# Kernel optimization log

Hardware: AMD Instinct MI355X
Metric: run time of the kernel (lower is better)

## Reference

```python
import math
import jax, jax.numpy as jnp
import numpy as np
from jax import lax

B, T, D = 2, 2048, 1024
H, W, E = 16, 16, 8
HD = D // H


def setup_inputs() -> dict:
    key = jax.random.key(0)
    ks = jax.random.split(key, 9)
    s = 0.02
    return {
        "x": jax.random.normal(ks[0], (B, T, D), dtype=jnp.float32),
        # CausalConv1d weights: torch Conv1d layout [out_ch, in_ch, kernel]
        "q_w": jax.random.normal(ks[1], (D, D, W), dtype=jnp.float32) * s,
        "q_b": jax.random.normal(ks[2], (D,), dtype=jnp.float32) * s,
        "k_w": jax.random.normal(ks[3], (D, D, W), dtype=jnp.float32) * s,
        "k_b": jax.random.normal(ks[4], (D,), dtype=jnp.float32) * s,
        # Linear weights: torch layout [out, in]
        "v_w": jax.random.normal(ks[5], (D, D), dtype=jnp.float32) * s,
        "v_b": jax.random.normal(ks[6], (D,), dtype=jnp.float32) * s,
        "p_w": jax.random.normal(ks[7], (D, D), dtype=jnp.float32) * s,
        "p_b": jax.random.normal(ks[8], (D,), dtype=jnp.float32) * s,
    }


def _causal_conv(x_t, w, b):
    # x_t: [B, D, T]; left-pad by W-1 so output at t sees inputs <= t
    xp = jnp.pad(x_t, ((0, 0), (0, 0), (W - 1, 0)))
    y = lax.conv_general_dilated(xp, w, window_strides=(1,), padding="VALID",
                                 dimension_numbers=("NCH", "OIH", "NCH"))
    return y + b[None, :, None]


def _split_heads(z):
    # [B, T, D] -> [B, H, T, hd]
    return z.reshape(B, T, H, HD).transpose(0, 2, 1, 3)


def reference(x, q_w, q_b, k_w, k_b, v_w, v_b, p_w, p_b):
    x_t = x.transpose(0, 2, 1)  # [B, D, T]
    q = _split_heads(_causal_conv(x_t, q_w, q_b).transpose(0, 2, 1))
    k = _split_heads(_causal_conv(x_t, k_w, k_b).transpose(0, 2, 1))
    v = _split_heads(jnp.einsum("btd,od->bto", x, v_w) + v_b)
    scale = 1.0 / math.sqrt(HD)

    # ---- local window attention (unfold equivalent) ----
    # zero-pad keys/values W-1 steps to the left along T, gather sliding windows
    k_pad = jnp.pad(k, ((0, 0), (0, 0), (W - 1, 0), (0, 0)))
    v_pad = jnp.pad(v, ((0, 0), (0, 0), (W - 1, 0), (0, 0)))
    widx = jnp.arange(T)[:, None] + jnp.arange(W)[None, :]  # [T, W]
    patches_k = k_pad[:, :, widx]  # [B, H, T, W, hd]
    patches_v = v_pad[:, :, widx]  # [B, H, T, W, hd]
    attn_l = jax.nn.softmax(jnp.einsum("bhtd,bhtwd->bhtw", q, patches_k) * scale, axis=-1)
    out_l = jnp.einsum("bhtw,bhtwd->bhtd", attn_l, patches_v)

    # ---- exponential jumps: roll by 2^e (wrap-around, as in original) ----
    out_e = jnp.zeros_like(out_l)
    for e in range(E):
        shift = 2 ** e
        if shift >= T:
            break
        k_s = jnp.roll(k, -shift, axis=2)
        v_s = jnp.roll(v, -shift, axis=2)
        score = jnp.sum(q * k_s, axis=-1) * scale  # [B, H, T]
        alpha = jax.nn.softmax(score, axis=-1)[..., None]  # softmax over T (faithful)
        out_e = out_e + alpha * v_s

    out = (out_l + out_e).transpose(0, 2, 1, 3).reshape(B, T, D)
    return jnp.einsum("btd,od->bto", out, p_w) + p_b
```

## Files before the change

kernel.cpp:

```cpp
#include <hip/hip_runtime.h>
#include <cstdint>
#include <cstddef>

#define TSEQ 2048
#define DDIM 1024

typedef _Float16 f16;
typedef _Float16 f16x2 __attribute__((ext_vector_type(2)));
typedef _Float16 f16x4 __attribute__((ext_vector_type(4)));
typedef _Float16 f16x8 __attribute__((ext_vector_type(8)));
typedef float f32x4 __attribute__((ext_vector_type(4)));


__device__ __align__(16) static const unsigned char g_zero16[16] = {};

__device__ __forceinline__ void gload_lds16(const void* g, void* l) {
  __builtin_amdgcn_global_load_lds(
      (const __attribute__((address_space(1))) void*)g,
      (__attribute__((address_space(3))) void*)l, 16, 0, 0);
}

__global__ void cvt_all(const float* __restrict__ x, const float* __restrict__ vw,
                        const float* __restrict__ pw,
                        f16* __restrict__ xh, f16* __restrict__ vwh, f16* __restrict__ pwh) {
  int b = blockIdx.x;
  const float* src; f16* dst; int i;
  if (b < 4096)      { src = x;  dst = xh;  i = b * 256 + threadIdx.x; }
  else if (b < 5120) { src = vw; dst = vwh; i = (b - 4096) * 256 + threadIdx.x; }
  else               { src = pw; dst = pwh; i = (b - 5120) * 256 + threadIdx.x; }
  float4 v = ((const float4*)src)[i];
  f16x4 h = { (f16)v.x, (f16)v.y, (f16)v.z, (f16)v.w };
  ((f16x4*)dst)[i] = h;
}

__global__ __launch_bounds__(256) void cvt_w_frag(const float* __restrict__ qw,
                                                  const float* __restrict__ kw,
                                                  f16* __restrict__ qd, f16* __restrict__ kd) {
  extern __shared__ f16 wt_lds[];
  const int bid = blockIdx.x;
  const int proj = bid >> 9;
  const int nb = (bid >> 5) & 15;
  const int j = (bid >> 3) & 3;
  const int ic = bid & 7;
  const float* src = proj ? kw : qw;
  f16* dst = proj ? kd : qd;
  const int o_base = nb * 64 + j * 16;
  const int tid = threadIdx.x;
  const int lane = tid & 63;
  const int wv = tid >> 6;

  #pragma unroll
  for (int p = 0; p < 32; p++) {
    const int gidx = p * 256 + tid;
    const int o_r = gidx >> 9;
    const int i_r = (gidx >> 2) & 127;
    const int wq2 = gidx & 3;
    float4 v = *(const float4*)(src + (size_t)(o_base + o_r) * 16384 +
                                (size_t)(ic * 128 + i_r) * 16 + wq2 * 4);
    const int g = i_r >> 3;
    const int gp = (g & 8) | ((g & 7) ^ (o_r & 7));
    const int ip = gp * 8 + (i_r & 7);
    f16* t0 = wt_lds + ((wq2 * 4) * 16 + o_r) * 130 + ip;
    t0[0]    = (f16)v.x;
    t0[2080] = (f16)v.y;
    t0[4160] = (f16)v.z;
    t0[6240] = (f16)v.w;
  }
  __syncthreads();

  const int o = lane & 15;
  const int lhi = lane >> 4;
  #pragma unroll
  for (int u4 = 0; u4 < 16; u4++) {
    const int u = u4 * 4 + wv;
    const int w = u >> 2, ih = (u >> 1) & 1, s = u & 1;
    const int gl = ih * 8 + s * 4 + lhi;
    const int gp = (gl & 8) | ((gl & 7) ^ (o & 7));
    f16x8 val = *(const f16x8*)&wt_lds[(w * 16 + o) * 130 + gp * 8];
    const size_t unit = ((size_t)(nb * 256 + (ic * 2 + ih) * 16 + w) * 8) + j * 2 + s;
    *(f16x8*)(dst + unit * 512 + lane * 8) = val;
  }
}

__global__ __launch_bounds__(512, 1) void gemm_qk8(
    const f16* __restrict__ xh,
    const f16* __restrict__ Wfq, const f16* __restrict__ Wfk,
    const float* __restrict__ bq, const float* __restrict__ bk,
    f16* __restrict__ oq, f16* __restrict__ ok)
{
  extern __shared__ __align__(16) f16 smem[];
  const int tid = threadIdx.x;
  const int lane = tid & 63;
  const int wid = tid >> 6;
  const int wq = wid >> 1;
  const int wp = wid & 1;

  const int flat = blockIdx.y * 16 + blockIdx.x;
  const int xcd = flat & 7;
  const int idx = flat >> 3;
  const int nblk = xcd * 2 + (idx >> 4);
  const int mblk = idx & 15;
  const int m0 = mblk * 256;
  const int n0 = nblk * 64;
  const int bT = m0 & ~(TSEQ - 1);
  const int t0 = m0 & (TSEQ - 1);

  const int srow = lane >> 3;
  const int chunk8 = (((lane & 7) ^ (srow & 7)) << 3);

  const f16* Wf = wp ? Wfk : Wfq;
  const f16* wbase = Wf + ((size_t)nblk << 20) + lane * 8;

  f32x4 acc[4][4] = {};
  f16x8 bfr[2][8];
  f16x8 afr[2][8];

  auto stageX = [&](int ib2, int bufp) {
    f16* sb = smem + bufp * 17408;
    const int ic = ib2 * 64 + chunk8;
    #pragma unroll
    for (int c = 0; c < 5; c++) {
      const int g = c * 8 + wid;
      if (g < 34) {
        const int srcT = t0 + g * 8 + srow - 15;
        const void* gp = (srcT >= 0)
            ? (const void*)(xh + (((size_t)(bT + srcT)) << 10) + ic)
            : (const void*)g_zero16;
        gload_lds16(gp, (void*)&sb[g * 512]);
      }
    }
  };

  auto loadB = [&](int kt, f16x8* bf) {
    const f16* p = wbase + ((size_t)kt << 12);
    #pragma unroll
    for (int f = 0; f < 8; f++)
      bf[f] = *(const f16x8*)(p + f * 512);
  };

  auto readA = [&](const f16* xb, int wt, f16x8* af) {
    const int rx = ((lane & 7) + wt) & 7;
    const int sl0 = (((lane >> 4)) ^ rx) << 3;
    const int sl1 = (((lane >> 4) + 4) ^ rx) << 3;
    #pragma unroll
    for (int i = 0; i < 4; i++) {
      const int row = wq * 64 + i * 16 + (lane & 15) + wt;
      af[i]     = *(const f16x8*)&xb[row * 64 + sl0];
      af[4 + i] = *(const f16x8*)&xb[row * 64 + sl1];
    }
  };

  stageX(0, 0);
  loadB(0, bfr[0]);
  asm volatile("s_waitcnt vmcnt(0)" ::: "memory");
  __builtin_amdgcn_s_barrier();
  __builtin_amdgcn_sched_barrier(0);

  for (int ib = 0; ib < 16; ib++) {
    if (ib > 0) {
      __builtin_amdgcn_s_barrier();
      __builtin_amdgcn_sched_barrier(0);
    }
    if (ib + 1 < 16) stageX(ib + 1, (ib + 1) & 1);
    __builtin_amdgcn_sched_barrier(0);
    const f16* xb = smem + (ib & 1) * 17408;
    readA(xb, 0, afr[0]);
    #pragma unroll
    for (int wt = 0; wt < 16; wt++) {
      if (wt < 15) readA(xb, wt + 1, afr[(wt + 1) & 1]);
      const int kt = ib * 16 + wt;
      if (kt + 1 < 256) loadB(kt + 1, bfr[(wt & 1) ^ 1]);
      __builtin_amdgcn_s_setprio(1);
      #pragma unroll
      for (int i = 0; i < 4; i++)
        #pragma unroll
        for (int j = 0; j < 4; j++)
          acc[i][j] = __builtin_amdgcn_mfma_f32_16x16x32_f16(
              afr[wt & 1][i], bfr[wt & 1][2 * j], acc[i][j], 0, 0, 0);
      #pragma unroll
      for (int i = 0; i < 4; i++)
        #pragma unroll
        for (int j = 0; j < 4; j++)
          acc[i][j] = __builtin_amdgcn_mfma_f32_16x16x32_f16(
              afr[wt & 1][4 + i], bfr[wt & 1][2 * j + 1], acc[i][j], 0, 0, 0);
      __builtin_amdgcn_s_setprio(0);
    }
  }

  const int crow = (lane >> 4) << 2;
  const int ccol = lane & 15;
  const int hh = n0 >> 6;
  const float* bias = wp ? bk : bq;
  f16* outp = wp ? ok : oq;
  #pragma unroll
  for (int j = 0; j < 4; j++) {
    const int col = n0 + j * 16 + ccol;
    const float bvl = bias[col];
    const int d = (j << 4) + ccol;
    #pragma unroll
    for (int i = 0; i < 4; i++) {
      #pragma unroll
      for (int r = 0; r < 4; r++) {
        const int row = m0 + wq * 64 + i * 16 + crow + r;
        const int b = row >> 11, t = row & (TSEQ - 1);
        outp[((size_t)(b * 16 + hh) * TSEQ + t) * 64 + d] = (f16)(acc[i][j][r] + bvl);
      }
    }
  }
}

template<int MODE>
__global__ __launch_bounds__(256, 2) void gemm_small(
    const f16* __restrict__ A, const f16* __restrict__ Bw,
    const float* __restrict__ bias, f16* __restrict__ oh, float* __restrict__ ofp)
{
  __shared__ f16 As[128 * 32];
  __shared__ f16 Bs[128 * 32];
  const int tid = threadIdx.x;
  const int lane = tid & 63;
  const int wid = tid >> 6;
  const int m0 = blockIdx.x * 128;
  const int n0 = blockIdx.y * 128;

  const int srow = lane >> 2;
  const int scg = ((lane & 3) ^ ((lane >> 3) & 3)) * 8;
  const int wm = wid & 1;
  const int wn = wid >> 1;

  f32x4 acc[4][4] = {};

  for (int kk = 0; kk < 1024; kk += 32) {
    __syncthreads();
    if (wid < 2) {
      #pragma unroll
      for (int c = 0; c < 4; c++) {
        const int r = wid * 64 + c * 16 + srow;
        const void* g = (const void*)(A + (((size_t)(m0 + r)) << 10) + kk + scg);
        gload_lds16(g, (void*)&As[(wid * 64 + c * 16) * 32]);
      }
    } else {
      #pragma unroll
      for (int c = 0; c < 4; c++) {
        const int r = (wid - 2) * 64 + c * 16 + srow;
        const void* g = (const void*)(Bw + (((size_t)(n0 + r)) << 10) + kk + scg);
        gload_lds16(g, (void*)&Bs[((wid - 2) * 64 + c * 16) * 32]);
      }
    }
    __syncthreads();
    const int koff = ((lane >> 4) ^ ((lane >> 1) & 3)) * 8;
    f16x8 af[4], bf[4];
    #pragma unroll
    for (int i = 0; i < 4; i++) {
      af[i] = *(const f16x8*)&As[(wm * 64 + i * 16 + (lane & 15)) * 32 + koff];
      bf[i] = *(const f16x8*)&Bs[(wn * 64 + i * 16 + (lane & 15)) * 32 + koff];
    }
    #pragma unroll
    for (int i = 0; i < 4; i++)
      #pragma unroll
      for (int j = 0; j < 4; j++)
        acc[i][j] = __builtin_amdgcn_mfma_f32_16x16x32_f16(af[i], bf[j], acc[i][j], 0, 0, 0);
  }

  const int crow = (lane >> 4) * 4;
  const int ccol = lane & 15;
  #pragma unroll
  for (int j = 0; j < 4; j++) {
    const int col = n0 + wn * 64 + j * 16 + ccol;
    const float bvl = bias[col];
    #pragma unroll
    for (int i = 0; i < 4; i++) {
      #pragma unroll
      for (int r = 0; r < 4; r++) {
        const int row = m0 + wm * 64 + i * 16 + crow + r;
        const float val = acc[i][j][r] + bvl;
        if (MODE == 1) {
          ofp[(size_t)row * DDIM + col] = val;
        } else {
          const int b = row >> 11, t = row & (TSEQ - 1);
          const int h = col >> 6, d = col & 63;
          oh[((size_t)(b * 16 + h) * TSEQ + t) * 64 + d] = (f16)val;
        }
      }
    }
  }
}

__global__ __launch_bounds__(256) void score_k(const f16* __restrict__ qh,
                                               const f16* __restrict__ kh,
                                               float* __restrict__ scores) {
  const int bid = blockIdx.x;
  const int bh = bid >> 5, tc = bid & 31;
  const int tid = threadIdx.x;
  const int wave = tid >> 6, lane = tid & 63;
  const int tr = lane >> 3, dc = lane & 7;
  const size_t base = ((size_t)bh) << 17;
  const f16* qb = qh + base;
  const f16* kb = kh + base;

  #pragma unroll
  for (int p = 0; p < 2; p++) {
    const int t = tc * 64 + p * 32 + wave * 8 + tr;
    f16x8 qv = *(const f16x8*)(qb + (size_t)t * 64 + dc * 8);
    const f16x2* qp = (const f16x2*)&qv;
    #pragma unroll
    for (int e = 0; e < 8; e++) {
      const int ts = (t + (1 << e)) & (TSEQ - 1);
      f16x8 kv = *(const f16x8*)(kb + (size_t)ts * 64 + dc * 8);
      const f16x2* kp = (const f16x2*)&kv;
      float s = 0.f;
      #pragma unroll
      for (int j = 0; j < 4; j++) s = __builtin_amdgcn_fdot2(qp[j], kp[j], s, false);
      s += __shfl_xor(s, 1, 64);
      s += __shfl_xor(s, 2, 64);
      s += __shfl_xor(s, 4, 64);
      if (dc == 0) scores[((size_t)(bh * 8 + e) << 11) + t] = s * 0.125f;
    }
  }
}

__global__ void softmax_k(float* __restrict__ scores) {
  __shared__ float red[4];
  int row = blockIdx.x;
  float* p = scores + ((size_t)row << 11);
  int tid = threadIdx.x;
  float v[8];
  float4 a = ((const float4*)p)[tid * 2];
  float4 b = ((const float4*)p)[tid * 2 + 1];
  v[0] = a.x; v[1] = a.y; v[2] = a.z; v[3] = a.w;
  v[4] = b.x; v[5] = b.y; v[6] = b.z; v[7] = b.w;
  float m = v[0];
  #pragma unroll
  for (int j = 1; j < 8; j++) m = fmaxf(m, v[j]);
  for (int o = 32; o > 0; o >>= 1) m = fmaxf(m, __shfl_xor(m, o, 64));
  if ((tid & 63) == 0) red[tid >> 6] = m;
  __syncthreads();
  m = fmaxf(fmaxf(red[0], red[1]), fmaxf(red[2], red[3]));
  __syncthreads();
  float s = 0.f;
  #pragma unroll
  for (int j = 0; j < 8; j++) { v[j] = __expf(v[j] - m); s += v[j]; }
  for (int o = 32; o > 0; o >>= 1) s += __shfl_xor(s, o, 64);
  if ((tid & 63) == 0) red[tid >> 6] = s;
  __syncthreads();
  s = (red[0] + red[1]) + (red[2] + red[3]);
  float inv = 1.0f / s;
  float4 o1 = make_float4(v[0] * inv, v[1] * inv, v[2] * inv, v[3] * inv);
  float4 o2 = make_float4(v[4] * inv, v[5] * inv, v[6] * inv, v[7] * inv);
  ((float4*)p)[tid * 2] = o1;
  ((float4*)p)[tid * 2 + 1] = o2;
}

__global__ __launch_bounds__(256) void attn_out_k(
    const f16* __restrict__ qh, const f16* __restrict__ kh, const f16* __restrict__ vh,
    const float* __restrict__ alpha, f16* __restrict__ outh)
{
  __shared__ f16 qL[64 * 64];
  __shared__ f16 kL[80 * 64];
  __shared__ f16 vL[208 * 64];
  __shared__ float scL[64 * 16];
  __shared__ float aL[8 * 64];
  const int bh = blockIdx.x, tc = blockIdx.y;
  const int t0 = tc * 64;
  const int tid = threadIdx.x;
  const size_t base = ((size_t)bh) << 17;

  for (int idx = tid; idx < 64 * 8; idx += 256) {
    int r = idx >> 3, c = idx & 7, sl = c ^ (r & 7);
    *(uint4*)&qL[r * 64 + sl * 8] = *(const uint4*)(qh + base + (size_t)(t0 + r) * 64 + c * 8);
  }
  for (int idx = tid; idx < 79 * 8; idx += 256) {
    int r = idx >> 3, c = idx & 7, sl = c ^ (r & 7);
    int g = t0 - 15 + r;
    uint4 val = (g < 0) ? make_uint4(0, 0, 0, 0)
                        : *(const uint4*)(kh + base + (size_t)g * 64 + c * 8);
    *(uint4*)&kL[r * 64 + sl * 8] = val;
  }
  for (int idx = tid; idx < 207 * 8; idx += 256) {
    int r = idx >> 3, c = idx & 7, sl = c ^ (r & 7);
    int g = t0 - 15 + r;
    uint4 val;
    if (g < 0) val = make_uint4(0, 0, 0, 0);
    else {
      if (g >= TSEQ) g -= TSEQ;
      val = *(const uint4*)(vh + base + (size_t)g * 64 + c * 8);
    }
    *(uint4*)&vL[r * 64 + sl * 8] = val;
  }
  for (int idx = tid; idx < 512; idx += 256) {
    int e = idx >> 6, i = idx & 63;
    aL[e * 64 + i] = alpha[((size_t)(bh * 8 + e) << 11) + t0 + i];
  }
  __syncthreads();

  {
    const int tl = tid & 63;
    const int wg = tid >> 6;
    f16x8 qv[8];
    #pragma unroll
    for (int c = 0; c < 8; c++) qv[c] = *(const f16x8*)&qL[tl * 64 + ((c ^ (tl & 7)) * 8)];
    const f16x2* qp = (const f16x2*)&qv[0];
    #pragma unroll
    for (int wi = 0; wi < 4; wi++) {
      const int w = wg * 4 + wi;
      const int r = tl + w;
      float s = 0.f;
      #pragma unroll
      for (int c = 0; c < 8; c++) {
        f16x8 kv = *(const f16x8*)&kL[r * 64 + ((c ^ (r & 7)) * 8)];
        const f16x2* kp = (const f16x2*)&kv;
        #pragma unroll
        for (int j = 0; j < 4; j++) s = __builtin_amdgcn_fdot2(qp[c * 4 + j], kp[j], s, false);
      }
      scL[tl * 16 + w] = s * 0.125f;
    }
  }
  __syncthreads();

  if (tid < 64) {
    float sc[16];
    float m = -1e30f;
    #pragma unroll
    for (int w = 0; w < 16; w++) { sc[w] = scL[tid * 16 + w]; m = fmaxf(m, sc[w]); }
    float sum = 0.f;
    #pragma unroll
    for (int w = 0; w < 16; w++) { sc[w] = __expf(sc[w] - m); sum += sc[w]; }
    float inv = 1.0f / sum;
    #pragma unroll
    for (int w = 0; w < 16; w++) scL[tid * 16 + w] = sc[w] * inv;
  }
  __syncthreads();

  {
    const int tl = tid >> 2;
    const int qd = tid & 3;
    float accv[16] = {};
    #pragma unroll
    for (int w = 0; w < 16; w++) {
      const float pw_ = scL[tl * 16 + w];
      const int r = tl + w;
      #pragma unroll
      for (int c2 = 0; c2 < 2; c2++) {
        const int c = qd * 2 + c2;
        f16x8 v = *(const f16x8*)&vL[r * 64 + ((c ^ (r & 7)) * 8)];
        #pragma unroll
        for (int j = 0; j < 8; j++) accv[c2 * 8 + j] += pw_ * (float)v[j];
      }
    }
    #pragma unroll
    for (int e = 0; e < 8; e++) {
      const float a = aL[e * 64 + tl];
      const int r = tl + 15 + (1 << e);
      #pragma unroll
      for (int c2 = 0; c2 < 2; c2++) {
        const int c = qd * 2 + c2;
        f16x8 v = *(const f16x8*)&vL[r * 64 + ((c ^ (r & 7)) * 8)];
        #pragma unroll
        for (int j = 0; j < 8; j++) accv[c2 * 8 + j] += a * (float)v[j];
      }
    }
    const int b = bh >> 4, h = bh & 15;
    f16* orow = outh + ((size_t)(b * TSEQ + t0 + tl)) * DDIM + h * 64 + qd * 16;
    #pragma unroll
    for (int c2 = 0; c2 < 2; c2++) {
      f16x8 v;
      #pragma unroll
      for (int j = 0; j < 8; j++) v[j] = (f16)accv[c2 * 8 + j];
      *(f16x8*)(orow + c2 * 8) = v;
    }
  }
}

extern "C" void kernel_launch(void* const* d_in, const int* in_sizes, int n_in,
                              void* d_out, int out_size, void* d_ws, size_t ws_size,
                              hipStream_t stream) {
  (void)in_sizes; (void)n_in; (void)out_size; (void)ws_size;
  const float* x   = (const float*)d_in[0];
  const float* q_w = (const float*)d_in[1];
  const float* q_b = (const float*)d_in[2];
  const float* k_w = (const float*)d_in[3];
  const float* k_b = (const float*)d_in[4];
  const float* v_w = (const float*)d_in[5];
  const float* v_b = (const float*)d_in[6];
  const float* p_w = (const float*)d_in[7];
  const float* p_b = (const float*)d_in[8];
  float* out = (float*)d_out;

  char* ws = (char*)d_ws;
  f16* xh      = (f16*)(ws);
  f16* qwh     = (f16*)(ws + 8388608);
  f16* kwh     = (f16*)(ws + 41943040);
  f16* vwh     = (f16*)(ws + 75497472);
  f16* pwh     = (f16*)(ws + 77594624);
  f16* qh      = (f16*)(ws + 79691776);
  f16* kh      = (f16*)(ws + 88080384);
  f16* vh      = (f16*)(ws + 96468992);
  f16* outh    = (f16*)(ws + 104857600);
  float* alpha = (float*)(ws + 113246208);

  static int s_attr_done = 0;
  if (!s_attr_done) {
    hipFuncSetAttribute((const void*)gemm_qk8,
                        hipFuncAttributeMaxDynamicSharedMemorySize, 69632);
    hipFuncSetAttribute((const void*)cvt_w_frag,
                        hipFuncAttributeMaxDynamicSharedMemorySize, 66560);
    s_attr_done = 1;
  }

  cvt_all<<<6144, 256, 0, stream>>>(x, v_w, p_w, xh, vwh, pwh);
  cvt_w_frag<<<1024, 256, 66560, stream>>>(q_w, k_w, qwh, kwh);

  gemm_qk8<<<dim3(16, 16), 512, 69632, stream>>>(xh, qwh, kwh, q_b, k_b, qh, kh);
  gemm_small<0><<<dim3(32, 8), 256, 0, stream>>>(xh, vwh, v_b, vh, nullptr);

  score_k<<<1024, 256, 0, stream>>>(qh, kh, alpha);
  softmax_k<<<256, 256, 0, stream>>>(alpha);
  attn_out_k<<<dim3(32, 32), 256, 0, stream>>>(qh, kh, vh, alpha, outh);

  gemm_small<1><<<dim3(32, 8), 256, 0, stream>>>(outh, pwh, p_b, nullptr, out);
}
```

Measured before the change: 509.2 us.

## Fuse V projection into QK conv GEMM and double-buffer small GEMM

Computes the V linear projection inside the Q/K causal-conv GEMM. It reuses the already-staged x tile at the tap-15 (zero-shift) window, using V weights pre-swizzled into fragment order by a new conversion kernel. This removes the separate V GEMM launch and its re-read of x, at the cost of extra accumulator registers and extra MFMAs on the Q-path waves. The remaining small GEMM (output projection) now double-buffers its LDS tiles to overlap global loads with MFMA.

```diff
diff --git a/kernel.cpp b/kernel.cpp
--- a/kernel.cpp
+++ b/kernel.cpp
@@ -20,17 +20,35 @@
       (__attribute__((address_space(3))) void*)l, 16, 0, 0);
 }
 
-__global__ void cvt_all(const float* __restrict__ x, const float* __restrict__ vw,
-                        const float* __restrict__ pw,
-                        f16* __restrict__ xh, f16* __restrict__ vwh, f16* __restrict__ pwh) {
+__global__ void cvt_all(const float* __restrict__ x, const float* __restrict__ pw,
+                        f16* __restrict__ xh, f16* __restrict__ pwh) {
   int b = blockIdx.x;
   const float* src; f16* dst; int i;
-  if (b < 4096)      { src = x;  dst = xh;  i = b * 256 + threadIdx.x; }
-  else if (b < 5120) { src = vw; dst = vwh; i = (b - 4096) * 256 + threadIdx.x; }
-  else               { src = pw; dst = pwh; i = (b - 5120) * 256 + threadIdx.x; }
+  if (b < 4096) { src = x;  dst = xh;  i = b * 256 + threadIdx.x; }
+  else          { src = pw; dst = pwh; i = (b - 4096) * 256 + threadIdx.x; }
   float4 v = ((const float4*)src)[i];
   f16x4 h = { (f16)v.x, (f16)v.y, (f16)v.z, (f16)v.w };
   ((f16x4*)dst)[i] = h;
+}
+
+__global__ __launch_bounds__(256) void cvt_vw_frag(const float* __restrict__ vw,
+                                                   f16* __restrict__ dst) {
+  const int nb = blockIdx.x >> 4, ib = blockIdx.x & 15;
+  const int tid = threadIdx.x;
+  #pragma unroll
+  for (int h = 0; h < 2; h++) {
+    const int u = h * 256 + tid;
+    const int f = u >> 6, l = u & 63;
+    const int j = f >> 1, s = f & 1;
+    const int o = nb * 64 + j * 16 + (l & 15);
+    const int i0 = ib * 64 + s * 32 + (l >> 4) * 8;
+    const float* p = vw + (size_t)o * 1024 + i0;
+    float4 a = *(const float4*)p;
+    float4 b = *(const float4*)(p + 4);
+    f16x8 v = { (f16)a.x, (f16)a.y, (f16)a.z, (f16)a.w,
+                (f16)b.x, (f16)b.y, (f16)b.z, (f16)b.w };
+    *(f16x8*)(dst + ((size_t)((nb * 16 + ib) * 8 + f)) * 512 + l * 8) = v;
+  }
 }
 
 __global__ __launch_bounds__(256) void cvt_w_frag(const float* __restrict__ qw,
@@ -84,9 +102,9 @@
 
 __global__ __launch_bounds__(512, 1) void gemm_qk8(
     const f16* __restrict__ xh,
-    const f16* __restrict__ Wfq, const f16* __restrict__ Wfk,
-    const float* __restrict__ bq, const float* __restrict__ bk,
-    f16* __restrict__ oq, f16* __restrict__ ok)
+    const f16* __restrict__ Wfq, const f16* __restrict__ Wfk, const f16* __restrict__ Wfv,
+    const float* __restrict__ bq, const float* __restrict__ bk, const float* __restrict__ bv,
+    f16* __restrict__ oq, f16* __restrict__ ok, f16* __restrict__ ov)
 {
   extern __shared__ __align__(16) f16 smem[];
   const int tid = threadIdx.x;
@@ -110,10 +128,13 @@
 
   const f16* Wf = wp ? Wfk : Wfq;
   const f16* wbase = Wf + ((size_t)nblk << 20) + lane * 8;
+  const f16* vbase = Wfv + ((size_t)nblk << 16) + lane * 8;
 
   f32x4 acc[4][4] = {};
+  f32x4 vacc[4][4] = {};
   f16x8 bfr[2][8];
   f16x8 afr[2][8];
+  f16x8 vf[8];
 
   auto stageX = [&](int ib2, int bufp) {
     f16* sb = smem + bufp * 17408;
@@ -138,6 +159,13 @@
       bf[f] = *(const f16x8*)(p + f * 512);
   };
 
+  auto loadV = [&](int ib2, f16x8* bf) {
+    const f16* p = vbase + ((size_t)ib2 << 12);
+    #pragma unroll
+    for (int f = 0; f < 8; f++)
+      bf[f] = *(const f16x8*)(p + f * 512);
+  };
+
   auto readA = [&](const f16* xb, int wt, f16x8* af) {
     const int rx = ((lane & 7) + wt) & 7;
     const int sl0 = (((lane >> 4)) ^ rx) << 3;
@@ -170,6 +198,7 @@
       if (wt < 15) readA(xb, wt + 1, afr[(wt + 1) & 1]);
       const int kt = ib * 16 + wt;
       if (kt + 1 < 256) loadB(kt + 1, bfr[(wt & 1) ^ 1]);
+      if (wt == 15 && wp == 0) loadV(ib, vf);
       __builtin_amdgcn_s_setprio(1);
       #pragma unroll
       for (int i = 0; i < 4; i++)
@@ -184,6 +213,22 @@
           acc[i][j] = __builtin_amdgcn_mfma_f32_16x16x32_f16(
               afr[wt & 1][4 + i], bfr[wt & 1][2 * j + 1], acc[i][j], 0, 0, 0);
       __builtin_amdgcn_s_setprio(0);
+      if (wt == 15 && wp == 0) {
+        __builtin_amdgcn_s_setprio(1);
+        #pragma unroll
+        for (int i = 0; i < 4; i++)
+          #pragma unroll
+          for (int j = 0; j < 4; j++)
+            vacc[i][j] = __builtin_amdgcn_mfma_f32_16x16x32_f16(
+                afr[1][i], vf[2 * j], vacc[i][j], 0, 0, 0);
+        #pragma unroll
+        for (int i = 0; i < 4; i++)
+          #pragma unroll
+          for (int j = 0; j < 4; j++)
+            vacc[i][j] = __builtin_amdgcn_mfma_f32_16x16x32_f16(
+                afr[1][4 + i], vf[2 * j + 1], vacc[i][j], 0, 0, 0);
+        __builtin_amdgcn_s_setprio(0);
+      }
     }
   }
 
@@ -207,6 +252,23 @@
       }
     }
   }
+  if (wp == 0) {
+    #pragma unroll
+    for (int j = 0; j < 4; j++) {
+      const int col = n0 + j * 16 + ccol;
+      const float bvl = bv[col];
+      const int d = (j << 4) + ccol;
+      #pragma unroll
+      for (int i = 0; i < 4; i++) {
+        #pragma unroll
+        for (int r = 0; r < 4; r++) {
+          const int row = m0 + wq * 64 + i * 16 + crow + r;
+          const int b = row >> 11, t = row & (TSEQ - 1);
+          ov[((size_t)(b * 16 + hh) * TSEQ + t) * 64 + d] = (f16)(vacc[i][j][r] + bvl);
+        }
+      }
+    }
+  }
 }
 
 template<int MODE>
@@ -214,8 +276,8 @@
     const f16* __restrict__ A, const f16* __restrict__ Bw,
     const float* __restrict__ bias, f16* __restrict__ oh, float* __restrict__ ofp)
 {
-  __shared__ f16 As[128 * 32];
-  __shared__ f16 Bs[128 * 32];
+  __shared__ f16 As[2][128 * 32];
+  __shared__ f16 Bs[2][128 * 32];
   const int tid = threadIdx.x;
   const int lane = tid & 63;
   const int wid = tid >> 6;
@@ -229,36 +291,46 @@
 
   f32x4 acc[4][4] = {};
 
-  for (int kk = 0; kk < 1024; kk += 32) {
-    __syncthreads();
+  auto stage = [&](int kk, int buf) {
     if (wid < 2) {
       #pragma unroll
       for (int c = 0; c < 4; c++) {
         const int r = wid * 64 + c * 16 + srow;
         const void* g = (const void*)(A + (((size_t)(m0 + r)) << 10) + kk + scg);
-        gload_lds16(g, (void*)&As[(wid * 64 + c * 16) * 32]);
+        gload_lds16(g, (void*)&As[buf][(wid * 64 + c * 16) * 32]);
       }
     } else {
       #pragma unroll
       for (int c = 0; c < 4; c++) {
         const int r = (wid - 2) * 64 + c * 16 + srow;
         const void* g = (const void*)(Bw + (((size_t)(n0 + r)) << 10) + kk + scg);
-        gload_lds16(g, (void*)&Bs[((wid - 2) * 64 + c * 16) * 32]);
-      }
-    }
-    __syncthreads();
+        gload_lds16(g, (void*)&Bs[buf][((wid - 2) * 64 + c * 16) * 32]);
+      }
+    }
+  };
+
+  stage(0, 0);
+  asm volatile("s_waitcnt vmcnt(0)" ::: "memory");
+  __syncthreads();
+
+  int buf = 0;
+  for (int it = 0; it < 32; it++) {
+    if (it + 1 < 32) stage((it + 1) * 32, buf ^ 1);
     const int koff = ((lane >> 4) ^ ((lane >> 1) & 3)) * 8;
     f16x8 af[4], bf[4];
     #pragma unroll
     for (int i = 0; i < 4; i++) {
-      af[i] = *(const f16x8*)&As[(wm * 64 + i * 16 + (lane & 15)) * 32 + koff];
-      bf[i] = *(const f16x8*)&Bs[(wn * 64 + i * 16 + (lane & 15)) * 32 + koff];
+      af[i] = *(const f16x8*)&As[buf][(wm * 64 + i * 16 + (lane & 15)) * 32 + koff];
+      bf[i] = *(const f16x8*)&Bs[buf][(wn * 64 + i * 16 + (lane & 15)) * 32 + koff];
     }
     #pragma unroll
     for (int i = 0; i < 4; i++)
       #pragma unroll
       for (int j = 0; j < 4; j++)
         acc[i][j] = __builtin_amdgcn_mfma_f32_16x16x32_f16(af[i], bf[j], acc[i][j], 0, 0, 0);
+    asm volatile("s_waitcnt vmcnt(0)" ::: "memory");
+    __syncthreads();
+    buf ^= 1;
   }
 
   const int crow = (lane >> 4) * 4;
@@ -506,11 +578,12 @@
     s_attr_done = 1;
   }
 
-  cvt_all<<<6144, 256, 0, stream>>>(x, v_w, p_w, xh, vwh, pwh);
+  cvt_all<<<5120, 256, 0, stream>>>(x, p_w, xh, pwh);
+  cvt_vw_frag<<<256, 256, 0, stream>>>(v_w, vwh);
   cvt_w_frag<<<1024, 256, 66560, stream>>>(q_w, k_w, qwh, kwh);
 
-  gemm_qk8<<<dim3(16, 16), 512, 69632, stream>>>(xh, qwh, kwh, q_b, k_b, qh, kh);
-  gemm_small<0><<<dim3(32, 8), 256, 0, stream>>>(xh, vwh, v_b, vh, nullptr);
+  gemm_qk8<<<dim3(16, 16), 512, 69632, stream>>>(xh, qwh, kwh, vwh,
+                                                 q_b, k_b, v_b, qh, kh, vh);
 
   score_k<<<1024, 256, 0, stream>>>(qh, kh, alpha);
   softmax_k<<<256, 256, 0, stream>>>(alpha);
```

Measured after the change: 619.1 us. 1.22x slower.

## Double-buffer LDS in small GEMM and drop A-fragment prefetch in conv GEMM

Applied to the files above, without the earlier changes.

The small V/P projection GEMM gains a second LDS buffer, so the next K-tile is loaded directly to LDS while MFMAs run on the current one, with a single barrier per iteration instead of two. The conv GEMM stops prefetching A fragments one step ahead into a double register buffer and reads them from LDS just before use. This lowers register pressure, but the LDS read latency is now exposed to the compiler's scheduling. Doubling the LDS in the small GEMM may lower occupancy slightly.

```diff
diff --git a/kernel.cpp b/kernel.cpp
--- a/kernel.cpp
+++ b/kernel.cpp
@@ -113,7 +113,6 @@
 
   f32x4 acc[4][4] = {};
   f16x8 bfr[2][8];
-  f16x8 afr[2][8];
 
   auto stageX = [&](int ib2, int bufp) {
     f16* sb = smem + bufp * 17408;
@@ -138,18 +137,6 @@
       bf[f] = *(const f16x8*)(p + f * 512);
   };
 
-  auto readA = [&](const f16* xb, int wt, f16x8* af) {
-    const int rx = ((lane & 7) + wt) & 7;
-    const int sl0 = (((lane >> 4)) ^ rx) << 3;
-    const int sl1 = (((lane >> 4) + 4) ^ rx) << 3;
-    #pragma unroll
-    for (int i = 0; i < 4; i++) {
-      const int row = wq * 64 + i * 16 + (lane & 15) + wt;
-      af[i]     = *(const f16x8*)&xb[row * 64 + sl0];
-      af[4 + i] = *(const f16x8*)&xb[row * 64 + sl1];
-    }
-  };
-
   stageX(0, 0);
   loadB(0, bfr[0]);
   asm volatile("s_waitcnt vmcnt(0)" ::: "memory");
@@ -164,11 +151,19 @@
     if (ib + 1 < 16) stageX(ib + 1, (ib + 1) & 1);
     __builtin_amdgcn_sched_barrier(0);
     const f16* xb = smem + (ib & 1) * 17408;
-    readA(xb, 0, afr[0]);
     #pragma unroll
     for (int wt = 0; wt < 16; wt++) {
-      if (wt < 15) readA(xb, wt + 1, afr[(wt + 1) & 1]);
       const int kt = ib * 16 + wt;
+      const int rx = ((lane & 7) + wt) & 7;
+      const int sl0 = (((lane >> 4)) ^ rx) << 3;
+      const int sl1 = (((lane >> 4) + 4) ^ rx) << 3;
+      f16x8 af[8];
+      #pragma unroll
+      for (int i = 0; i < 4; i++) {
+        const int row = wq * 64 + i * 16 + (lane & 15) + wt;
+        af[i]     = *(const f16x8*)&xb[row * 64 + sl0];
+        af[4 + i] = *(const f16x8*)&xb[row * 64 + sl1];
+      }
       if (kt + 1 < 256) loadB(kt + 1, bfr[(wt & 1) ^ 1]);
       __builtin_amdgcn_s_setprio(1);
       #pragma unroll
@@ -176,13 +171,13 @@
         #pragma unroll
         for (int j = 0; j < 4; j++)
           acc[i][j] = __builtin_amdgcn_mfma_f32_16x16x32_f16(
-              afr[wt & 1][i], bfr[wt & 1][2 * j], acc[i][j], 0, 0, 0);
+              af[i], bfr[wt & 1][2 * j], acc[i][j], 0, 0, 0);
       #pragma unroll
       for (int i = 0; i < 4; i++)
         #pragma unroll
         for (int j = 0; j < 4; j++)
           acc[i][j] = __builtin_amdgcn_mfma_f32_16x16x32_f16(
-              afr[wt & 1][4 + i], bfr[wt & 1][2 * j + 1], acc[i][j], 0, 0, 0);
+              af[4 + i], bfr[wt & 1][2 * j + 1], acc[i][j], 0, 0, 0);
       __builtin_amdgcn_s_setprio(0);
     }
   }
@@ -214,8 +209,8 @@
     const f16* __restrict__ A, const f16* __restrict__ Bw,
     const float* __restrict__ bias, f16* __restrict__ oh, float* __restrict__ ofp)
 {
-  __shared__ f16 As[128 * 32];
-  __shared__ f16 Bs[128 * 32];
+  __shared__ f16 As[2][128 * 32];
+  __shared__ f16 Bs[2][128 * 32];
   const int tid = threadIdx.x;
   const int lane = tid & 63;
   const int wid = tid >> 6;
@@ -229,36 +224,46 @@
 
   f32x4 acc[4][4] = {};
 
-  for (int kk = 0; kk < 1024; kk += 32) {
-    __syncthreads();
+  auto stage = [&](int kk, int buf) {
     if (wid < 2) {
       #pragma unroll
       for (int c = 0; c < 4; c++) {
         const int r = wid * 64 + c * 16 + srow;
         const void* g = (const void*)(A + (((size_t)(m0 + r)) << 10) + kk + scg);
-        gload_lds16(g, (void*)&As[(wid * 64 + c * 16) * 32]);
+        gload_lds16(g, (void*)&As[buf][(wid * 64 + c * 16) * 32]);
       }
     } else {
       #pragma unroll
       for (int c = 0; c < 4; c++) {
         const int r = (wid - 2) * 64 + c * 16 + srow;
         const void* g = (const void*)(Bw + (((size_t)(n0 + r)) << 10) + kk + scg);
-        gload_lds16(g, (void*)&Bs[((wid - 2) * 64 + c * 16) * 32]);
-      }
-    }
-    __syncthreads();
+        gload_lds16(g, (void*)&Bs[buf][((wid - 2) * 64 + c * 16) * 32]);
+      }
+    }
+  };
+
+  stage(0, 0);
+  asm volatile("s_waitcnt vmcnt(0)" ::: "memory");
+  __syncthreads();
+
+  int buf = 0;
+  for (int it = 0; it < 32; it++) {
+    if (it + 1 < 32) stage((it + 1) * 32, buf ^ 1);
     const int koff = ((lane >> 4) ^ ((lane >> 1) & 3)) * 8;
     f16x8 af[4], bf[4];
     #pragma unroll
     for (int i = 0; i < 4; i++) {
-      af[i] = *(const f16x8*)&As[(wm * 64 + i * 16 + (lane & 15)) * 32 + koff];
-      bf[i] = *(const f16x8*)&Bs[(wn * 64 + i * 16 + (lane & 15)) * 32 + koff];
+      af[i] = *(const f16x8*)&As[buf][(wm * 64 + i * 16 + (lane & 15)) * 32 + koff];
+      bf[i] = *(const f16x8*)&Bs[buf][(wn * 64 + i * 16 + (lane & 15)) * 32 + koff];
     }
     #pragma unroll
     for (int i = 0; i < 4; i++)
       #pragma unroll
       for (int j = 0; j < 4; j++)
         acc[i][j] = __builtin_amdgcn_mfma_f32_16x16x32_f16(af[i], bf[j], acc[i][j], 0, 0, 0);
+    asm volatile("s_waitcnt vmcnt(0)" ::: "memory");
+    __syncthreads();
+    buf ^= 1;
   }
 
   const int crow = (lane >> 4) * 4;
```

After: 475.1 us. 1.07x faster.
